# Kernel tuning notes

Hardware: AMD Instinct MI355X
Metric: run time of the kernel (lower is better)

Reference implementation:

```python
import jax, jax.numpy as jnp
import numpy as np

U, D_IN, RANK, N = 128, 10240, 320, 32

def setup_inputs() -> dict:
    key = jax.random.key(0)
    ks = jax.random.split(key, 9)
    s = 0.02
    return {
        "x": jax.random.normal(ks[0], (U, D_IN), jnp.float32),
        "h": jax.random.normal(ks[1], (U, D_IN, N), jnp.float32),
        "W_delta": jax.random.normal(ks[2], (D_IN, RANK), jnp.float32) * s,
        "W_dt": jax.random.normal(ks[3], (RANK, D_IN), jnp.float32) * s,
        "b_dt": jax.random.normal(ks[4], (D_IN,), jnp.float32) * s,
        "W_B": jax.random.normal(ks[5], (D_IN, N), jnp.float32) * s,
        "W_C": jax.random.normal(ks[6], (D_IN, N), jnp.float32) * s,
        # A = -exp(A_log): strictly negative, so exp(delta*A) in (0,1)
        "A": -jnp.exp(jax.random.normal(ks[7], (D_IN, N), jnp.float32) * 0.5),
        "D": jax.random.normal(ks[8], (D_IN,), jnp.float32),
    }

def reference(x, h, W_delta, W_dt, b_dt, W_B, W_C, A, D):
    # dt projection: low-rank then up-proj + bias, softplus (beta=1, threshold=20)
    delta = jax.nn.softplus(x @ W_delta @ W_dt + b_dt)          # [U, D_IN]
    # B and C input-dependent projections
    B = x @ W_B                                                  # [U, N]
    C = x @ W_C                                                  # [U, N]
    # discretize: abar = exp(delta * A); bbar*x = delta * B * x
    abar = jnp.exp(delta[:, :, None] * A[None, :, :])            # [U, D_IN, N]
    bx = (delta * x)[:, :, None] * B[:, None, :]                 # [U, D_IN, N]
    h_new = abar * h + bx                                        # state update
    # output: y_d = sum_n h[d,n] * C[n] + D_d * x_d
    y = jnp.einsum('udn,un->ud', h_new, C) + D[None, :] * x      # [U, D_IN]
    return y, h_new
```

## Files before the change

kernel.cpp:

```cpp
#include <hip/hip_runtime.h>

#define U_    128
#define DIN   10240
#define RANK  320
#define NS    32
#define NTOT  384

__global__ __launch_bounds__(256) void transpose_kernel(
    const float* __restrict__ x, float* __restrict__ xT)
{
    __shared__ float tile[32][33];
    int kb = blockIdx.x * 32, ub = blockIdx.y * 32;
    int tx = threadIdx.x, ty = threadIdx.y;
#pragma unroll
    for (int i = 0; i < 32; i += 8)
        tile[ty + i][tx] = x[(size_t)(ub + ty + i) * DIN + kb + tx];
    __syncthreads();
#pragma unroll
    for (int i = 0; i < 32; i += 8)
        xT[(size_t)(kb + ty + i) * U_ + ub + tx] = tile[tx][ty + i];
}

template<int KCC>
__global__ __launch_bounds__(128) void gemmA_kernel(
    const float* __restrict__ xT,
    const float* __restrict__ Wd, const float* __restrict__ Wb,
    const float* __restrict__ Wc,
    float* __restrict__ partial)
{
    int b     = blockIdx.x;
    int kc_lo = b & 7;
    int rest  = b >> 3;
    int nt    = rest % 12;
    int kc    = (rest / 12) * 8 + kc_lo;
    int u     = threadIdx.x;
    int n0    = nt * 32;

    const float* W; int ldw, c0;
    if (nt < 10)       { W = Wd; ldw = RANK; c0 = n0; }
    else if (nt == 10) { W = Wb; ldw = NS;   c0 = 0;  }
    else               { W = Wc; ldw = NS;   c0 = 0;  }

    float acc[32];
#pragma unroll
    for (int j = 0; j < 32; ++j) acc[j] = 0.f;

    constexpr int KCHUNK = DIN / KCC;
    int k0 = kc * KCHUNK;
    const float* Wp = W  + (size_t)k0 * ldw + c0;
    const float* xp = xT + (size_t)k0 * U_ + u;

#pragma unroll 4
    for (int k = 0; k < KCHUNK; ++k) {
        float xv = xp[(size_t)k * U_];
#pragma unroll
        for (int j = 0; j < 32; ++j)
            acc[j] += xv * Wp[(size_t)k * ldw + j];
    }

    float* out = partial + (size_t)kc * (NTOT * U_) + (size_t)n0 * U_ + u;
#pragma unroll
    for (int j = 0; j < 32; ++j)
        out[(size_t)j * U_] = acc[j];
}

template<int KCC>
__global__ __launch_bounds__(256) void reduce_kernel(
    const float* __restrict__ partial, float* __restrict__ tT,
    float* __restrict__ Bc, float* __restrict__ Cc)
{
    int e = blockIdx.x * 256 + threadIdx.x;
    float s = 0.f;
#pragma unroll 8
    for (int kc = 0; kc < KCC; ++kc)
        s += partial[(size_t)kc * (NTOT * U_) + e];
    int n = e >> 7, u = e & 127;
    if (n < RANK)            tT[e] = s;
    else if (n < RANK + NS)  Bc[u * NS + (n - RANK)] = s;
    else                     Cc[u * NS + (n - RANK - NS)] = s;
}

__global__ __launch_bounds__(64) void delta_kernel(
    const float* __restrict__ tT, const float* __restrict__ Wdt,
    const float* __restrict__ b_dt, float* __restrict__ delta)
{
    int b   = blockIdx.x;
    int dt_ = b % 160, ut = b / 160;
    int d   = dt_ * 64 + threadIdx.x;
    int u0  = ut * 16;

    float bias = b_dt[d];
    float acc[16];
#pragma unroll
    for (int i = 0; i < 16; ++i) acc[i] = bias;

#pragma unroll 4
    for (int r = 0; r < RANK; ++r) {
        float w = Wdt[(size_t)r * DIN + d];
        const float* tp = tT + r * U_ + u0;
#pragma unroll
        for (int i = 0; i < 16; ++i)
            acc[i] += w * tp[i];
    }
#pragma unroll
    for (int i = 0; i < 16; ++i) {
        float z = acc[i];
        float sp = (z > 20.f) ? z : log1pf(__expf(z));
        delta[(size_t)(u0 + i) * DIN + d] = sp;
    }
}

__global__ __launch_bounds__(256) void ssm_kernel(
    const float* __restrict__ x, const float* __restrict__ h,
    const float* __restrict__ delta,
    const float* __restrict__ Bc, const float* __restrict__ Cc,
    const float* __restrict__ A, const float* __restrict__ Dvec,
    float* __restrict__ y, float* __restrict__ hnew)
{
    int idx4 = blockIdx.x * 256 + threadIdx.x;
    int n4 = idx4 & 7;
    int ud = idx4 >> 3;
    int d = ud % DIN;
    int u = ud / DIN;

    float dlt = delta[ud];
    float xv  = x[ud];

    float4 hv = ((const float4*)h)[idx4];
    float4 av = ((const float4*)A)[(size_t)d * 8 + n4];
    float4 bv = ((const float4*)Bc)[u * 8 + n4];
    float4 cv = ((const float4*)Cc)[u * 8 + n4];

    float dx = dlt * xv;
    float4 hn;
    hn.x = __expf(dlt * av.x) * hv.x + dx * bv.x;
    hn.y = __expf(dlt * av.y) * hv.y + dx * bv.y;
    hn.z = __expf(dlt * av.z) * hv.z + dx * bv.z;
    hn.w = __expf(dlt * av.w) * hv.w + dx * bv.w;

    ((float4*)hnew)[idx4] = hn;

    float p = hn.x * cv.x + hn.y * cv.y + hn.z * cv.z + hn.w * cv.w;
    p += __shfl_xor(p, 4, 8);
    p += __shfl_xor(p, 2, 8);
    p += __shfl_xor(p, 1, 8);
    if (n4 == 0)
        y[ud] = p + Dvec[d] * xv;
}

extern "C" void kernel_launch(void* const* d_in, const int* in_sizes, int n_in,
                              void* d_out, int out_size, void* d_ws, size_t ws_size,
                              hipStream_t stream)
{
    const float* x   = (const float*)d_in[0];
    const float* h   = (const float*)d_in[1];
    const float* Wd  = (const float*)d_in[2];
    const float* Wdt = (const float*)d_in[3];
    const float* bdt = (const float*)d_in[4];
    const float* Wb  = (const float*)d_in[5];
    const float* Wc  = (const float*)d_in[6];
    const float* A   = (const float*)d_in[7];
    const float* Dv  = (const float*)d_in[8];

    const bool big = ws_size >= (size_t)4505600 * 4;
    const size_t partial_elems = (size_t)(big ? 64 : 32) * NTOT * U_;

    float* ws      = (float*)d_ws;
    float* xT      = ws;
    float* partial = ws + 1310720;
    float* delta   = partial;
    float* tT      = partial + partial_elems;
    float* Bc      = tT + 40960;
    float* Cc      = Bc + 4096;

    float* y    = (float*)d_out;
    float* hnew = y + (size_t)U_ * DIN;

    dim3 tb(32, 8);
    transpose_kernel<<<dim3(DIN / 32, U_ / 32), tb, 0, stream>>>(x, xT);
    if (big) {
        gemmA_kernel<64><<<12 * 64, 128, 0, stream>>>(xT, Wd, Wb, Wc, partial);
        reduce_kernel<64><<<192, 256, 0, stream>>>(partial, tT, Bc, Cc);
    } else {
        gemmA_kernel<32><<<12 * 32, 128, 0, stream>>>(xT, Wd, Wb, Wc, partial);
        reduce_kernel<32><<<192, 256, 0, stream>>>(partial, tT, Bc, Cc);
    }
    delta_kernel<<<1280, 64, 0, stream>>>(tT, Wdt, bdt, delta);
    ssm_kernel  <<<40960, 256, 0, stream>>>(x, h, delta, Bc, Cc, A, Dv, y, hnew);
}
```

Baseline: 412.0 us.

## Stage weights and low-rank activations in LDS for projection and delta GEMMs

The projection GEMM now loads its weight tile into shared memory with float4 loads and splits the K chunk across two halves of a 256-thread block, combining the partial sums through LDS. The delta kernel stages its tT slice in shared memory, uses 128 threads per block and covers 8 users per block instead of 16. Both changes target uncoalesced or scalar global reads of weights and activations in the small GEMMs, and add barriers and LDS traffic in exchange. The memory-bound SSM kernel, which dominates runtime, is unchanged.

```diff
diff --git a/kernel.cpp b/kernel.cpp
--- a/kernel.cpp
+++ b/kernel.cpp
@@ -22,46 +22,72 @@
 }
 
 template<int KCC>
-__global__ __launch_bounds__(128) void gemmA_kernel(
+__global__ __launch_bounds__(256) void gemmA_kernel(
     const float* __restrict__ xT,
     const float* __restrict__ Wd, const float* __restrict__ Wb,
     const float* __restrict__ Wc,
     float* __restrict__ partial)
 {
-    int b     = blockIdx.x;
-    int kc_lo = b & 7;
-    int rest  = b >> 3;
-    int nt    = rest % 12;
-    int kc    = (rest / 12) * 8 + kc_lo;
-    int u     = threadIdx.x;
-    int n0    = nt * 32;
+    constexpr int KCH   = DIN / KCC;
+    constexpr int KHALF = KCH / 2;
+    __shared__ float Wl[KCH][32];
+
+    int b  = blockIdx.x;
+    int nt = b / KCC;
+    int kc = b % KCC;
+    int n0 = nt * 32;
+    int k0 = kc * KCH;
 
     const float* W; int ldw, c0;
     if (nt < 10)       { W = Wd; ldw = RANK; c0 = n0; }
     else if (nt == 10) { W = Wb; ldw = NS;   c0 = 0;  }
     else               { W = Wc; ldw = NS;   c0 = 0;  }
 
+    for (int i4 = threadIdx.x; i4 < KCH * 8; i4 += 256) {
+        int r = i4 >> 3;
+        int c = (i4 & 7) * 4;
+        *(float4*)&Wl[r][c] =
+            *(const float4*)&W[(size_t)(k0 + r) * ldw + c0 + c];
+    }
+    __syncthreads();
+
+    int u    = threadIdx.x & 127;
+    int half = threadIdx.x >> 7;
+
     float acc[32];
 #pragma unroll
     for (int j = 0; j < 32; ++j) acc[j] = 0.f;
 
-    constexpr int KCHUNK = DIN / KCC;
-    int k0 = kc * KCHUNK;
-    const float* Wp = W  + (size_t)k0 * ldw + c0;
-    const float* xp = xT + (size_t)k0 * U_ + u;
-
-#pragma unroll 4
-    for (int k = 0; k < KCHUNK; ++k) {
+    const float* xp = xT + (size_t)(k0 + half * KHALF) * U_ + u;
+    int kbase = half * KHALF;
+
+#pragma unroll 8
+    for (int k = 0; k < KHALF; ++k) {
         float xv = xp[(size_t)k * U_];
+        const float4* wr = (const float4*)&Wl[kbase + k][0];
+#pragma unroll
+        for (int j4 = 0; j4 < 8; ++j4) {
+            float4 w = wr[j4];
+            acc[j4 * 4 + 0] += xv * w.x;
+            acc[j4 * 4 + 1] += xv * w.y;
+            acc[j4 * 4 + 2] += xv * w.z;
+            acc[j4 * 4 + 3] += xv * w.w;
+        }
+    }
+
+    __syncthreads();
+    float* comb = &Wl[0][0];
+    if (half == 1) {
+#pragma unroll
+        for (int j = 0; j < 32; ++j) comb[j * 128 + u] = acc[j];
+    }
+    __syncthreads();
+    if (half == 0) {
+        float* out = partial + (size_t)kc * (NTOT * U_) + (size_t)n0 * U_ + u;
 #pragma unroll
         for (int j = 0; j < 32; ++j)
-            acc[j] += xv * Wp[(size_t)k * ldw + j];
-    }
-
-    float* out = partial + (size_t)kc * (NTOT * U_) + (size_t)n0 * U_ + u;
-#pragma unroll
-    for (int j = 0; j < 32; ++j)
-        out[(size_t)j * U_] = acc[j];
+            out[(size_t)j * U_] = acc[j] + comb[j * 128 + u];
+    }
 }
 
 template<int KCC>
@@ -80,30 +106,39 @@
     else                     Cc[u * NS + (n - RANK - NS)] = s;
 }
 
-__global__ __launch_bounds__(64) void delta_kernel(
+__global__ __launch_bounds__(128) void delta_kernel(
     const float* __restrict__ tT, const float* __restrict__ Wdt,
     const float* __restrict__ b_dt, float* __restrict__ delta)
 {
+    __shared__ float ts[RANK][8];
     int b   = blockIdx.x;
-    int dt_ = b % 160, ut = b / 160;
-    int d   = dt_ * 64 + threadIdx.x;
-    int u0  = ut * 16;
+    int dt_ = b % 80, ut = b / 80;
+    int d   = dt_ * 128 + threadIdx.x;
+    int u0  = ut * 8;
+
+    for (int i4 = threadIdx.x; i4 < RANK * 2; i4 += 128) {
+        int r = i4 >> 1, c = (i4 & 1) * 4;
+        *(float4*)&ts[r][c] = *(const float4*)&tT[(size_t)r * U_ + u0 + c];
+    }
+    __syncthreads();
 
     float bias = b_dt[d];
-    float acc[16];
-#pragma unroll
-    for (int i = 0; i < 16; ++i) acc[i] = bias;
+    float acc[8];
+#pragma unroll
+    for (int i = 0; i < 8; ++i) acc[i] = bias;
 
 #pragma unroll 4
     for (int r = 0; r < RANK; ++r) {
         float w = Wdt[(size_t)r * DIN + d];
-        const float* tp = tT + r * U_ + u0;
-#pragma unroll
-        for (int i = 0; i < 16; ++i)
-            acc[i] += w * tp[i];
-    }
-#pragma unroll
-    for (int i = 0; i < 16; ++i) {
+        const float4* tp = (const float4*)&ts[r][0];
+        float4 t0 = tp[0], t1 = tp[1];
+        acc[0] += w * t0.x; acc[1] += w * t0.y;
+        acc[2] += w * t0.z; acc[3] += w * t0.w;
+        acc[4] += w * t1.x; acc[5] += w * t1.y;
+        acc[6] += w * t1.z; acc[7] += w * t1.w;
+    }
+#pragma unroll
+    for (int i = 0; i < 8; ++i) {
         float z = acc[i];
         float sp = (z > 20.f) ? z : log1pf(__expf(z));
         delta[(size_t)(u0 + i) * DIN + d] = sp;
@@ -179,12 +214,12 @@
     dim3 tb(32, 8);
     transpose_kernel<<<dim3(DIN / 32, U_ / 32), tb, 0, stream>>>(x, xT);
     if (big) {
-        gemmA_kernel<64><<<12 * 64, 128, 0, stream>>>(xT, Wd, Wb, Wc, partial);
+        gemmA_kernel<64><<<12 * 64, 256, 0, stream>>>(xT, Wd, Wb, Wc, partial);
         reduce_kernel<64><<<192, 256, 0, stream>>>(partial, tT, Bc, Cc);
     } else {
-        gemmA_kernel<32><<<12 * 32, 128, 0, stream>>>(xT, Wd, Wb, Wc, partial);
+        gemmA_kernel<32><<<12 * 32, 256, 0, stream>>>(xT, Wd, Wb, Wc, partial);
         reduce_kernel<32><<<192, 256, 0, stream>>>(partial, tT, Bc, Cc);
     }
-    delta_kernel<<<1280, 64, 0, stream>>>(tT, Wdt, bdt, delta);
+    delta_kernel<<<80 * 16, 128, 0, stream>>>(tT, Wdt, bdt, delta);
     ssm_kernel  <<<40960, 256, 0, stream>>>(x, h, delta, Bc, Cc, A, Dv, y, hnew);
 }
```

After: 391.6 us. 1.05x faster.
